# Kernel tuning notes

Measured on AMD Instinct MI355X. Metric: run time of the kernel, lower is better.

## Reference

```python
import jax, jax.numpy as jnp
import numpy as np

# Config mirroring the TF module: cross-attention path (one_on_rna == 2),
# use_attn_augument=1, aug_multiply=0, two_d_softm=1, two_d_softm_mul_row_count=1,
# reduce_level=20 (protok used for padding masks).
B, L, D, H = 4, 1024, 512, 8
DEPTH = D // H          # 64, matches the repeat(64) in padding_to_zeros
NEG = -1.0e9


def setup_inputs() -> dict:
    key = jax.random.key(0)
    ks = jax.random.split(key, 16)
    s = np.float32(1.0 / np.sqrt(D))  # glorot-ish scale
    q = jax.random.normal(ks[0], (B, L, D), jnp.float32)
    kv = jax.random.normal(ks[1], (B, L, D), jnp.float32)
    # protein tokens; 0 == padding (compared against 0.0 in the TF code)
    protok = jax.random.randint(ks[2], (B, L), 0, 21).astype(jnp.float32)
    statpot_hb = jax.random.uniform(ks[3], (B, L, L), dtype=jnp.float32)
    statpot_pi = jax.random.uniform(ks[4], (B, L, L), dtype=jnp.float32)
    # cross padding mask: 1.0 where the protein (query) position is padding
    pad = (protok == 0.0).astype(jnp.float32)            # [B, L]
    cross_mask = jnp.broadcast_to(pad[:, :, None], (B, L, L)).astype(jnp.float32)
    wq = jax.random.normal(ks[5], (D, D), jnp.float32) * s
    wk = jax.random.normal(ks[6], (D, D), jnp.float32) * s
    wv = jax.random.normal(ks[7], (D, D), jnp.float32) * s
    wo = jax.random.normal(ks[8], (D, D), jnp.float32) * s
    bq = jnp.zeros((D,), jnp.float32)
    bk = jnp.zeros((D,), jnp.float32)
    bv = jnp.zeros((D,), jnp.float32)
    bo = jnp.zeros((D,), jnp.float32)
    aug_weight_att = jnp.ones((1,), jnp.float32)
    aug_weight_aug = jnp.ones((1,), jnp.float32)
    return dict(q=q, kv=kv, protok=protok, statpot_hb=statpot_hb,
                statpot_pi=statpot_pi, cross_mask=cross_mask,
                wq=wq, bq=bq, wk=wk, bk=bk, wv=wv, bv=bv, wo=wo, bo=bo,
                aug_weight_att=aug_weight_att, aug_weight_aug=aug_weight_aug)


def _split_heads(x):
    # [B, L, D] -> [B, H, L, depth]
    return x.reshape(B, L, H, DEPTH).transpose(0, 2, 1, 3)


def reference(q, kv, protok, statpot_hb, statpot_pi, cross_mask,
              wq, bq, wk, bk, wv, bv, wo, bo, aug_weight_att, aug_weight_aug):
    # padding_to_zeros: zero features at padded protein positions
    pad_keep = (protok != 0.0).astype(q.dtype)[:, :, None]   # [B, L, 1]
    qp = (q @ wq + bq) * pad_keep   # query side is the protein (len == max_pro_len)
    k = kv @ wk + bk
    v = kv @ wv + bv
    qh, kh, vh = _split_heads(qp), _split_heads(k), _split_heads(v)

    # unscaled QK^T (original does NOT divide by sqrt(depth))
    logits = jnp.einsum('bhqd,bhkd->bhqk', qh, kh)           # [B,H,L,L]

    # statistical-potential augmentation (aug_multiply == 0 -> additive)
    table = jnp.stack([statpot_hb, statpot_pi], axis=1)      # [B,2,L,L]
    table = jnp.repeat(table, H // 2, axis=1)                # [B,H,L,L]
    logits = logits / jnp.max(logits)
    logits = aug_weight_att * logits
    table = aug_weight_aug * table
    table = table / jnp.max(table)
    logits = logits + table

    # additive large-negative mask, broadcast over heads
    logits = logits + cross_mask[:, None, :, :] * NEG

    # 2D softmax jointly over (query, key) axes
    attn = jax.nn.softmax(logits.reshape(B, H, L * L), axis=-1).reshape(B, H, L, L)

    # rescale by number of non-padded protein rows (two_d_softm_mul_row_count)
    mul = jnp.count_nonzero(protok, axis=1).astype(attn.dtype)[:, None, None, None]
    attn = attn * mul
    attn = attn / jnp.max(attn)

    # output = attn^T @ v : contracts the QUERY axis (as in the original matmul)
    out = jnp.einsum('bhqk,bhqd->bhkd', attn, vh)            # [B,H,L,depth]
    out = out.transpose(0, 2, 1, 3).reshape(B, L, D)
    out = out @ wo + bo
    out = out * pad_keep                                     # final padding zeroing
    return out
```

## Files before the change

### kernel.cpp

```cpp
#include <hip/hip_runtime.h>
#include <math.h>

#define BB 4
#define LL 1024
#define DD 512
#define HH 8
#define DEP 64
#define NEGV (-1.0e9f)

typedef __attribute__((ext_vector_type(8))) short bf16x8;
typedef __attribute__((ext_vector_type(4))) float f32x4;
typedef unsigned short u16;
typedef unsigned int u32;

#define S_TMAX 1
#define S_TMIN 2
#define S_MUL  4
#define S_SUM  8
#define S_M    40
#define P_TMAX 128
#define P_TMIN 384
#define P_GMAX 640
#define SCAL_F 1792
#define PER_T  (BB*HH*LL*DEP)

__device__ inline u16 f2b(float x) {
  u32 u = __float_as_uint(x);
  return (u16)((u + 0x7FFFu + ((u >> 16) & 1u)) >> 16);
}
__device__ inline float b2f(u16 h) { return __uint_as_float(((u32)h) << 16); }

__device__ inline void atomicMaxF(float* addr, float val) {
  unsigned int* ua = (unsigned int*)addr;
  unsigned int old = *ua;
  while (__uint_as_float(old) < val) {
    unsigned int assumed = old;
    old = atomicCAS(ua, assumed, __float_as_uint(val));
    if (old == assumed) break;
  }
}

__global__ __launch_bounds__(256) void k_tminmax(const float* __restrict__ hb,
                                                 const float* __restrict__ pi,
                                                 const float* __restrict__ protok,
                                                 float* __restrict__ ws) {
  const int t = threadIdx.x;
  if (blockIdx.x == 4 && t < 32) {
    ws[S_SUM + t] = 0.0f; ws[S_M + t] = -INFINITY;
  }
  if (blockIdx.x < 4) {
    int b = blockIdx.x;
    int cnt = 0;
    for (int l = t; l < LL; l += 256)
      cnt += (protok[b*LL + l] != 0.0f) ? 1 : 0;
    __shared__ int shc[4];
    int lane = t & 63, w = t >> 6;
    #pragma unroll
    for (int o = 32; o > 0; o >>= 1) cnt += __shfl_down(cnt, o);
    if (lane == 0) shc[w] = cnt;
    __syncthreads();
    if (t == 0) ws[S_MUL + b] = (float)(shc[0] + shc[1] + shc[2] + shc[3]);
  }
  const int g = blockIdx.x*256 + t;
  float mx = -INFINITY, mn = INFINITY;
  #pragma unroll
  for (int rep = 0; rep < 4; ++rep) {
    float4 a[4], c[4];
    #pragma unroll
    for (int j = 0; j < 4; ++j) {
      size_t idx = (size_t)rep*262144 + (size_t)j*65536 + g;
      a[j] = ((const float4*)hb)[idx];
      c[j] = ((const float4*)pi)[idx];
    }
    #pragma unroll
    for (int j = 0; j < 4; ++j) {
      mx = fmaxf(mx, fmaxf(fmaxf(a[j].x, a[j].y), fmaxf(a[j].z, a[j].w)));
      mx = fmaxf(mx, fmaxf(fmaxf(c[j].x, c[j].y), fmaxf(c[j].z, c[j].w)));
      mn = fminf(mn, fminf(fminf(a[j].x, a[j].y), fminf(a[j].z, a[j].w)));
      mn = fminf(mn, fminf(fminf(c[j].x, c[j].y), fminf(c[j].z, c[j].w)));
    }
  }
  __shared__ float shx[4], shn[4];
  int lane = t & 63, w = t >> 6;
  #pragma unroll
  for (int o = 32; o > 0; o >>= 1) {
    mx = fmaxf(mx, __shfl_down(mx, o));
    mn = fminf(mn, __shfl_down(mn, o));
  }
  if (lane == 0) { shx[w] = mx; shn[w] = mn; }
  __syncthreads();
  if (t == 0) {
    ws[P_TMAX + blockIdx.x] = fmaxf(fmaxf(shx[0], shx[1]), fmaxf(shx[2], shx[3]));
    ws[P_TMIN + blockIdx.x] = fminf(fminf(shn[0], shn[1]), fminf(shn[2], shn[3]));
  }
}

__global__ __launch_bounds__(256) void k_prep(
    const float* __restrict__ q, const float* __restrict__ kv,
    const float* __restrict__ wq, const float* __restrict__ wk,
    const float* __restrict__ wv, const float* __restrict__ wo,
    u16* __restrict__ Xb, u16* __restrict__ WTb, float* __restrict__ ws) {
  const int bid = blockIdx.x;
  const int t = threadIdx.x;
  if (bid < 2048) {
    int tg = bid*256 + t;
    int which = tg >> 18;
    size_t off8 = (size_t)(tg & 262143) * 8;
    const float* s = which ? kv : q;
    float4 f0 = *(const float4*)&s[off8];
    float4 f1 = *(const float4*)&s[off8 + 4];
    u32 p0 = (u32)f2b(f0.x) | ((u32)f2b(f0.y) << 16);
    u32 p1 = (u32)f2b(f0.z) | ((u32)f2b(f0.w) << 16);
    u32 p2 = (u32)f2b(f1.x) | ((u32)f2b(f1.y) << 16);
    u32 p3 = (u32)f2b(f1.z) | ((u32)f2b(f1.w) << 16);
    *(int4*)&Xb[(size_t)which*PER_T + off8] = make_int4(p0, p1, p2, p3);
  } else if (bid < 2304) {
    const int wid = bid - 2048;
    const int g = wid >> 6, rem = wid & 63;
    const int k0 = (rem >> 3)*64, n0 = (rem & 7)*64;
    const float* W = (g==0)?wq:(g==1)?wk:(g==2)?wv:wo;
    __shared__ u16 Ls[64][72];
    {
      const int r = t>>2, c16 = (t&3)*16;
      float v[16];
      #pragma unroll
      for (int j=0;j<4;++j) {
        float4 f = *(const float4*)&W[(size_t)(k0+r)*DD + n0 + c16 + 4*j];
        v[4*j]=f.x; v[4*j+1]=f.y; v[4*j+2]=f.z; v[4*j+3]=f.w;
      }
      u32 pk_[8];
      #pragma unroll
      for (int j=0;j<8;++j) pk_[j] = (u32)f2b(v[2*j]) | ((u32)f2b(v[2*j+1])<<16);
      *(int4*)&Ls[r][c16]   = make_int4(pk_[0],pk_[1],pk_[2],pk_[3]);
      *(int4*)&Ls[r][c16+8] = make_int4(pk_[4],pk_[5],pk_[6],pk_[7]);
    }
    __syncthreads();
    {
      const int n = t>>2, kk = (t&3)*16;
      u16 u[16];
      #pragma unroll
      for (int j=0;j<16;++j) u[j] = Ls[kk+j][n];
      u32 q_[8];
      #pragma unroll
      for (int j=0;j<8;++j) q_[j] = (u32)u[2*j] | ((u32)u[2*j+1]<<16);
      size_t dst = ((size_t)(g*DD + n0 + n))*DD + k0 + kk;
      *(int4*)&WTb[dst]   = make_int4(q_[0],q_[1],q_[2],q_[3]);
      *(int4*)&WTb[dst+8] = make_int4(q_[4],q_[5],q_[6],q_[7]);
    }
  } else {
    float tm = ws[P_TMAX + t];
    float tn = ws[P_TMIN + t];
    __shared__ float st[4], sn[4];
    int lane = t & 63, w = t >> 6;
    #pragma unroll
    for (int o = 32; o > 0; o >>= 1) {
      tm = fmaxf(tm, __shfl_down(tm, o));
      tn = fminf(tn, __shfl_down(tn, o));
    }
    if (lane == 0) { st[w] = tm; sn[w] = tn; }
    __syncthreads();
    if (t == 0) {
      ws[S_TMAX] = fmaxf(fmaxf(st[0], st[1]), fmaxf(st[2], st[3]));
      ws[S_TMIN] = fminf(fminf(sn[0], sn[1]), fminf(sn[2], sn[3]));
    }
  }
}

__global__ __launch_bounds__(256) void k1_proj(
    const float* __restrict__ protok,
    const float* __restrict__ bq, const float* __restrict__ bk,
    const float* __restrict__ bv,
    const u16* __restrict__ Xb, const u16* __restrict__ WTb,
    u16* __restrict__ QPb, u16* __restrict__ KHb, u16* __restrict__ VTb) {
  const int gid = blockIdx.z;
  const u16* X = Xb + (gid == 0 ? 0 : (size_t)PER_T);
  const float* bia = (gid == 0) ? bq : (gid == 1) ? bk : bv;
  const int m0 = blockIdx.x*64;
  const int h  = blockIdx.y;
  __shared__ u16 As[64][72];
  __shared__ u16 Bs[64][72];
  const int t = threadIdx.x;
  const int w = t>>6, lane = t&63, i = lane&15, g2 = lane>>4;
  const int sr = t>>2, sc = (t&3)*16;

  f32x4 acc[4];
  #pragma unroll
  for (int ct=0;ct<4;++ct) acc[ct] = (f32x4){0.f,0.f,0.f,0.f};

  for (int kk0 = 0; kk0 < DD; kk0 += 64) {
    __syncthreads();
    {
      size_t sx = (size_t)(m0+sr)*DD + kk0 + sc;
      *(int4*)&As[sr][sc]   = *(const int4*)&X[sx];
      *(int4*)&As[sr][sc+8] = *(const int4*)&X[sx+8];
    }
    {
      size_t src = ((size_t)(gid*DD + h*64 + sr))*DD + kk0 + sc;
      *(int4*)&Bs[sr][sc]   = *(const int4*)&WTb[src];
      *(int4*)&Bs[sr][sc+8] = *(const int4*)&WTb[src+8];
    }
    __syncthreads();
    bf16x8 a0 = *(const bf16x8*)&As[16*w + i][g2*8];
    bf16x8 a1 = *(const bf16x8*)&As[16*w + i][32 + g2*8];
    #pragma unroll
    for (int ct=0; ct<4; ++ct) {
      bf16x8 b0 = *(const bf16x8*)&Bs[ct*16 + i][g2*8];
      bf16x8 b1 = *(const bf16x8*)&Bs[ct*16 + i][32 + g2*8];
      acc[ct] = __builtin_amdgcn_mfma_f32_16x16x32_bf16(a0, b0, acc[ct], 0,0,0);
      acc[ct] = __builtin_amdgcn_mfma_f32_16x16x32_bf16(a1, b1, acc[ct], 0,0,0);
    }
  }
  __syncthreads();
  const int lrow = 16*w + g2*4;
  if (gid == 2) {
    #pragma unroll
    for (int ct=0;ct<4;++ct)
      #pragma unroll
      for (int r=0;r<4;++r)
        As[lrow + r][ct*16 + i] = f2b(acc[ct][r] + bia[h*64 + ct*16 + i]);
    __syncthreads();
    const int b = m0 >> 10, l0 = m0 & 1023;
    const int d = t>>2, lc = (t&3)*16;
    u16 u[16];
    #pragma unroll
    for (int j=0;j<16;++j) u[j] = As[lc+j][d];
    u32 q_[8];
    #pragma unroll
    for (int j=0;j<8;++j) q_[j] = (u32)u[2*j] | ((u32)u[2*j+1]<<16);
    size_t dst = ((size_t)(b*HH + h)*DEP + d)*LL + l0 + lc;
    *(int4*)&VTb[dst]   = make_int4(q_[0],q_[1],q_[2],q_[3]);
    *(int4*)&VTb[dst+8] = make_int4(q_[4],q_[5],q_[6],q_[7]);
  } else {
    u16* Y = (gid == 0) ? QPb : KHb;
    #pragma unroll
    for (int ct=0;ct<4;++ct)
      #pragma unroll
      for (int r=0;r<4;++r) {
        int m = m0 + lrow + r;
        float keep = (gid == 0) ? ((protok[m] != 0.0f) ? 1.0f : 0.0f) : 1.0f;
        int b = m >> 10, l = m & 1023;
        float val = (acc[ct][r] + bia[h*64 + ct*16 + i]) * keep;
        Y[((size_t)(b*HH + h)*LL + l)*DEP + ct*16 + i] = f2b(val);
      }
  }
}

__global__ __launch_bounds__(256) void k3_gmax(
    const u16* __restrict__ QPb, const u16* __restrict__ KHb,
    float* __restrict__ wsf) {
  const int q0 = blockIdx.x*128, bh = blockIdx.y, kz = blockIdx.z;
  __shared__ u16 Qs[2][64][72];
  __shared__ u16 Ks[2][64][72];
  const int t = threadIdx.x;
  const int w = t>>6, lane = t&63, i = lane&15, g2 = lane>>4;
  const int sr = t>>2, sc = (t&3)*16;
  const u16* Qb = QPb + (size_t)bh*LL*DEP;
  const u16* Kb = KHb + (size_t)bh*LL*DEP;
  #pragma unroll
  for (int qs = 0; qs < 2; ++qs) {
    size_t sq = (size_t)(q0 + qs*64 + sr)*DEP + sc;
    *(int4*)&Qs[qs][sr][sc]   = *(const int4*)&Qb[sq];
    *(int4*)&Qs[qs][sr][sc+8] = *(const int4*)&Qb[sq+8];
  }
  const int kb = kz*4;
  int4 rn0 = *(const int4*)&Kb[(size_t)(kb*64 + sr)*DEP + sc];
  int4 rn1 = *(const int4*)&Kb[(size_t)(kb*64 + sr)*DEP + sc + 8];
  __syncthreads();
  *(int4*)&Ks[0][sr][sc]   = rn0;
  *(int4*)&Ks[0][sr][sc+8] = rn1;
  rn0 = *(const int4*)&Kb[(size_t)((kb+1)*64 + sr)*DEP + sc];
  rn1 = *(const int4*)&Kb[(size_t)((kb+1)*64 + sr)*DEP + sc + 8];
  __syncthreads();
  bf16x8 a0[2], a1[2];
  #pragma unroll
  for (int qs = 0; qs < 2; ++qs) {
    a0[qs] = *(const bf16x8*)&Qs[qs][16*w + i][g2*8];
    a1[qs] = *(const bf16x8*)&Qs[qs][16*w + i][32 + g2*8];
  }
  float mx = -INFINITY;
  for (int kt = 0; kt < 4; ++kt) {
    const int cur = kt & 1;
    #pragma unroll
    for (int ct=0;ct<4;++ct) {
      bf16x8 b0 = *(const bf16x8*)&Ks[cur][ct*16 + i][g2*8];
      bf16x8 b1 = *(const bf16x8*)&Ks[cur][ct*16 + i][32 + g2*8];
      #pragma unroll
      for (int qs=0;qs<2;++qs) {
        f32x4 z = (f32x4){0.f,0.f,0.f,0.f};
        z = __builtin_amdgcn_mfma_f32_16x16x32_bf16(a0[qs], b0, z, 0,0,0);
        z = __builtin_amdgcn_mfma_f32_16x16x32_bf16(a1[qs], b1, z, 0,0,0);
        mx = fmaxf(mx, fmaxf(fmaxf(z[0],z[1]), fmaxf(z[2],z[3])));
      }
    }
    if (kt < 3) {
      __syncthreads();
      *(int4*)&Ks[cur^1][sr][sc]   = rn0;
      *(int4*)&Ks[cur^1][sr][sc+8] = rn1;
      if (kt < 2) {
        rn0 = *(const int4*)&Kb[(size_t)((kb+kt+2)*64 + sr)*DEP + sc];
        rn1 = *(const int4*)&Kb[(size_t)((kb+kt+2)*64 + sr)*DEP + sc + 8];
      }
      __syncthreads();
    }
  }
  __shared__ float red[4];
  #pragma unroll
  for (int o = 32; o > 0; o >>= 1) mx = fmaxf(mx, __shfl_down(mx, o));
  if (lane == 0) red[w] = mx;
  __syncthreads();
  if (t == 0)
    wsf[P_GMAX + (bh*8 + blockIdx.x)*4 + kz] =
        fmaxf(fmaxf(red[0],red[1]), fmaxf(red[2],red[3]));
}

__global__ __launch_bounds__(256) void k4_fused(
    const float* __restrict__ protok,
    const float* __restrict__ hb, const float* __restrict__ pi,
    const float* __restrict__ w_att, const float* __restrict__ w_aug,
    const u16* __restrict__ QPb, const u16* __restrict__ KHb,
    const u16* __restrict__ VTb,
    u16* __restrict__ Ob0, u16* __restrict__ Ob1,
    float* __restrict__ wsf) {
  const int k0 = blockIdx.x*64;
  const int bh = blockIdx.y, b = bh>>3, h = bh&7;
  const int qbase = blockIdx.z * 512;
  u16* Obz = blockIdx.z ? Ob1 : Ob0;
  const float* tab = ((h < 4) ? hb : pi) + (size_t)b*LL*LL;
  const int t = threadIdx.x;
  const int w = t>>6, lane = t&63, i = lane&15, g2 = lane>>4;
  const int sr = t>>2, sc = (t&3)*16;
  const int qlb = 16*w + g2*4;

  __shared__ float gsh;
  {
    float gm = -INFINITY;
    #pragma unroll
    for (int j=0;j<4;++j) gm = fmaxf(gm, wsf[P_GMAX + j*256 + t]);
    __shared__ float red[4];
    #pragma unroll
    for (int o = 32; o > 0; o >>= 1) gm = fmaxf(gm, __shfl_down(gm, o));
    if (lane == 0) red[w] = gm;
    __syncthreads();
    if (t == 0) gsh = fmaxf(fmaxf(red[0],red[1]), fmaxf(red[2],red[3]));
  }
  const float tmaxr = wsf[S_TMAX], tminr = wsf[S_TMIN];
  const float wa = w_att[0], wg = w_aug[0];
  const float tden = (wg >= 0.0f) ? (wg * tmaxr) : (wg * tminr);
  const float inv_t = wg / tden;

  __shared__ u16 Ks[64][72];
  __shared__ u16 Qs[64][72];
  __shared__ u16 Vt[64][72];
  __shared__ u16 Pt[64][72];
  {
    size_t sk = ((size_t)bh*LL + k0 + sr)*DEP + sc;
    *(int4*)&Ks[sr][sc]   = *(const int4*)&KHb[sk];
    *(int4*)&Ks[sr][sc+8] = *(const int4*)&KHb[sk+8];
  }
  int4 rq0 = *(const int4*)&QPb[((size_t)bh*LL + qbase + sr)*DEP + sc];
  int4 rq1 = *(const int4*)&QPb[((size_t)bh*LL + qbase + sr)*DEP + sc + 8];
  int4 rv0 = *(const int4*)&VTb[((size_t)bh*DEP + sr)*LL + qbase + sc];
  int4 rv1 = *(const int4*)&VTb[((size_t)bh*DEP + sr)*LL + qbase + sc + 8];
  float tvr[4][4];
  #pragma unroll
  for (int r=0;r<4;++r)
    #pragma unroll
    for (int ct=0;ct<4;++ct)
      tvr[r][ct] = tab[(size_t)(qbase + qlb + r)*LL + k0 + ct*16 + i];
  __syncthreads();
  const float inv_g = wa / gsh;
  bf16x8 kb0[4], kb1[4];
  #pragma unroll
  for (int ct=0;ct<4;++ct) {
    kb0[ct] = *(const bf16x8*)&Ks[ct*16 + i][g2*8];
    kb1[ct] = *(const bf16x8*)&Ks[ct*16 + i][32 + g2*8];
  }
  f32x4 accO[4];
  #pragma unroll
  for (int dt=0;dt<4;++dt) accO[dt] = (f32x4){0.f,0.f,0.f,0.f};
  float lsum = 0.0f, lmax = -INFINITY;

  for (int q0 = qbase; q0 < qbase + 512; q0 += 64) {
    const bool more = (q0 + 64) < (qbase + 512);
    __syncthreads();
    *(int4*)&Qs[sr][sc]   = rq0;
    *(int4*)&Qs[sr][sc+8] = rq1;
    *(int4*)&Vt[sr][sc]   = rv0;
    *(int4*)&Vt[sr][sc+8] = rv1;
    __syncthreads();
    if (more) {
      rq0 = *(const int4*)&QPb[((size_t)bh*LL + q0 + 64 + sr)*DEP + sc];
      rq1 = *(const int4*)&QPb[((size_t)bh*LL + q0 + 64 + sr)*DEP + sc + 8];
      rv0 = *(const int4*)&VTb[((size_t)bh*DEP + sr)*LL + q0 + 64 + sc];
      rv1 = *(const int4*)&VTb[((size_t)bh*DEP + sr)*LL + q0 + 64 + sc + 8];
    }
    bf16x8 a0 = *(const bf16x8*)&Qs[16*w + i][g2*8];
    bf16x8 a1 = *(const bf16x8*)&Qs[16*w + i][32 + g2*8];
    f32x4 s4[4];
    #pragma unroll
    for (int ct=0; ct<4; ++ct) {
      f32x4 z = (f32x4){0.f,0.f,0.f,0.f};
      z = __builtin_amdgcn_mfma_f32_16x16x32_bf16(a0, kb0[ct], z, 0,0,0);
      z = __builtin_amdgcn_mfma_f32_16x16x32_bf16(a1, kb1[ct], z, 0,0,0);
      s4[ct] = z;
    }
    float tv2[4][4];
    if (more) {
      #pragma unroll
      for (int r=0;r<4;++r)
        #pragma unroll
        for (int ct=0;ct<4;++ct)
          tv2[r][ct] = tab[(size_t)(q0 + 64 + qlb + r)*LL + k0 + ct*16 + i];
    }
    float madd[4];
    #pragma unroll
    for (int r=0;r<4;++r)
      madd[r] = (protok[b*LL + q0 + qlb + r] == 0.0f) ? NEGV : 0.0f;
    #pragma unroll
    for (int ct=0;ct<4;++ct) {
      float pr[4];
      #pragma unroll
      for (int r=0;r<4;++r) {
        float sp = fmaf(s4[ct][r], inv_g, fmaf(tvr[r][ct], inv_t, madd[r]));
        lmax = fmaxf(lmax, sp);
        float p = __expf(sp);
        lsum += p;
        pr[r] = p;
      }
      u32 pk0 = (u32)f2b(pr[0]) | ((u32)f2b(pr[1])<<16);
      u32 pk1 = (u32)f2b(pr[2]) | ((u32)f2b(pr[3])<<16);
      *(uint2*)&Pt[ct*16 + i][qlb] = make_uint2(pk0, pk1);
    }
    __syncthreads();
    bf16x8 pa0 = *(const bf16x8*)&Pt[16*w + i][g2*8];
    bf16x8 pa1 = *(const bf16x8*)&Pt[16*w + i][32 + g2*8];
    #pragma unroll
    for (int dt=0; dt<4; ++dt) {
      bf16x8 v0 = *(const bf16x8*)&Vt[dt*16 + i][g2*8];
      bf16x8 v1 = *(const bf16x8*)&Vt[dt*16 + i][32 + g2*8];
      accO[dt] = __builtin_amdgcn_mfma_f32_16x16x32_bf16(pa0, v0, accO[dt], 0,0,0);
      accO[dt] = __builtin_amdgcn_mfma_f32_16x16x32_bf16(pa1, v1, accO[dt], 0,0,0);
    }
    if (more) {
      #pragma unroll
      for (int r=0;r<4;++r)
        #pragma unroll
        for (int ct=0;ct<4;++ct) tvr[r][ct] = tv2[r][ct];
    }
  }
  #pragma unroll
  for (int dt=0;dt<4;++dt)
    #pragma unroll
    for (int r=0;r<4;++r)
      Obz[((size_t)bh*LL + k0 + qlb + r)*DEP + dt*16 + i] = f2b(accO[dt][r]);
  __shared__ float rs[4], rm[4];
  #pragma unroll
  for (int o = 32; o > 0; o >>= 1) {
    lsum += __shfl_down(lsum, o);
    lmax = fmaxf(lmax, __shfl_down(lmax, o));
  }
  if (lane == 0) { rs[w] = lsum; rm[w] = lmax; }
  __syncthreads();
  if (t == 0) {
    atomicAdd(&wsf[S_SUM + bh], rs[0]+rs[1]+rs[2]+rs[3]);
    atomicMaxF(&wsf[S_M + bh], fmaxf(fmaxf(rm[0], rm[1]), fmaxf(rm[2], rm[3])));
  }
}

__global__ __launch_bounds__(256) void k5_out(
    const float* __restrict__ protok,
    const float* __restrict__ bo,
    const u16* __restrict__ WTb,
    const u16* __restrict__ O0, const u16* __restrict__ O1,
    const float* __restrict__ wsf, float* __restrict__ out) {
  const int m0 = blockIdx.x*64, n0 = blockIdx.y*64;
  const int b = m0 >> 10, l0 = m0 & 1023;
  __shared__ u16 As[64][72];
  __shared__ u16 Bs[64][72];
  __shared__ float csh[8];
  const int t = threadIdx.x;
  const int w = t>>6, lane = t&63, i = lane&15, g2 = lane>>4;
  const int sr = t>>2, sc = (t&3)*16;

  __shared__ float ash[32];
  if (t < 32)
    ash[t] = wsf[S_MUL + (t>>3)] * __expf(wsf[S_M + t]) / wsf[S_SUM + t];
  __syncthreads();
  if (t < 8) {
    float amax = -INFINITY;
    #pragma unroll
    for (int j = 0; j < 32; ++j) amax = fmaxf(amax, ash[j]);
    csh[t] = (wsf[S_MUL + b] / wsf[S_SUM + b*HH + t]) / amax;
  }

  f32x4 acc[4];
  #pragma unroll
  for (int ct=0;ct<4;++ct) acc[ct] = (f32x4){0.f,0.f,0.f,0.f};

  for (int kk0 = 0; kk0 < DD; kk0 += 64) {
    const int h = kk0 >> 6;
    __syncthreads();
    {
      union { int4 v[2]; u16 u[16]; } u0, u1;
      size_t so = ((size_t)(b*HH + h)*LL + l0 + sr)*DEP + sc;
      u0.v[0] = *(const int4*)&O0[so];
      u0.v[1] = *(const int4*)&O0[so+8];
      u1.v[0] = *(const int4*)&O1[so];
      u1.v[1] = *(const int4*)&O1[so+8];
      const float cs = csh[h];
      u32 pk_[8];
      #pragma unroll
      for (int j=0;j<8;++j) {
        float lo = (b2f(u0.u[2*j])   + b2f(u1.u[2*j]))   * cs;
        float hi = (b2f(u0.u[2*j+1]) + b2f(u1.u[2*j+1])) * cs;
        pk_[j] = (u32)f2b(lo) | ((u32)f2b(hi)<<16);
      }
      *(int4*)&As[sr][sc]   = make_int4(pk_[0],pk_[1],pk_[2],pk_[3]);
      *(int4*)&As[sr][sc+8] = make_int4(pk_[4],pk_[5],pk_[6],pk_[7]);
    }
    {
      size_t src = ((size_t)(3*DD + n0 + sr))*DD + kk0 + sc;
      *(int4*)&Bs[sr][sc]   = *(const int4*)&WTb[src];
      *(int4*)&Bs[sr][sc+8] = *(const int4*)&WTb[src+8];
    }
    __syncthreads();
    bf16x8 a0 = *(const bf16x8*)&As[16*w + i][g2*8];
    bf16x8 a1 = *(const bf16x8*)&As[16*w + i][32 + g2*8];
    #pragma unroll
    for (int ct=0; ct<4; ++ct) {
      bf16x8 b0 = *(const bf16x8*)&Bs[ct*16 + i][g2*8];
      bf16x8 b1 = *(const bf16x8*)&Bs[ct*16 + i][32 + g2*8];
      acc[ct] = __builtin_amdgcn_mfma_f32_16x16x32_bf16(a0, b0, acc[ct], 0,0,0);
      acc[ct] = __builtin_amdgcn_mfma_f32_16x16x32_bf16(a1, b1, acc[ct], 0,0,0);
    }
  }
  #pragma unroll
  for (int ct=0;ct<4;++ct)
    #pragma unroll
    for (int r=0;r<4;++r) {
      int m = m0 + 16*w + g2*4 + r;
      float keep = (protok[m] != 0.0f) ? 1.0f : 0.0f;
      out[(size_t)m*DD + n0 + ct*16 + i] = (acc[ct][r] + bo[n0 + ct*16 + i]) * keep;
    }
}

extern "C" void kernel_launch(void* const* d_in, const int* in_sizes, int n_in,
                              void* d_out, int out_size, void* d_ws, size_t ws_size,
                              hipStream_t stream) {
  const float* q      = (const float*)d_in[0];
  const float* kv     = (const float*)d_in[1];
  const float* protok = (const float*)d_in[2];
  const float* hb     = (const float*)d_in[3];
  const float* pi     = (const float*)d_in[4];
  const float* wq = (const float*)d_in[6];
  const float* bq = (const float*)d_in[7];
  const float* wk = (const float*)d_in[8];
  const float* bk = (const float*)d_in[9];
  const float* wv = (const float*)d_in[10];
  const float* bv = (const float*)d_in[11];
  const float* wo = (const float*)d_in[12];
  const float* bo = (const float*)d_in[13];
  const float* w_att = (const float*)d_in[14];
  const float* w_aug = (const float*)d_in[15];
  float* wsf = (float*)d_ws;
  float* out = (float*)d_out;

  u16* base = (u16*)(wsf + SCAL_F);
  u16* QPb = base;
  u16* KHb = QPb + PER_T;
  u16* VTb = KHb + PER_T;
  u16* XO  = VTb + PER_T;
  u16* WTb = XO  + 2*PER_T;
  u16* Xb  = XO;
  u16* Ob0 = XO;
  u16* Ob1 = XO + PER_T;

  k_tminmax <<<256, 256, 0, stream>>>(hb, pi, protok, wsf);
  k_prep    <<<2305, 256, 0, stream>>>(q, kv, wq, wk, wv, wo, Xb, WTb, wsf);
  k1_proj   <<<dim3(64, 8, 3), 256, 0, stream>>>(protok, bq, bk, bv, Xb, WTb, QPb, KHb, VTb);
  k3_gmax   <<<dim3(8, 32, 4), 256, 0, stream>>>(QPb, KHb, wsf);
  k4_fused  <<<dim3(16, 32, 2), 256, 0, stream>>>(protok, hb, pi, w_att, w_aug,
                                                  QPb, KHb, VTb, Ob0, Ob1, wsf);
  k5_out    <<<dim3(64, 8), 256, 0, stream>>>(protok, bo, WTb, Ob0, Ob1, wsf, out);
}
```

Measured before the change: 215.3 us.

## Fuse table min/max into prep, drop LDS staging, unsplit query axis in attention

Merges the table min/max and row-count kernel into the prep kernel, which removes one launch and moves the final min/max reduction into the attention kernel. The projection and global-max kernels now load MFMA operands straight from global memory instead of staging them in LDS with barriers. The fused attention kernel stops splitting the query axis into two halves, so it writes a single output buffer and the output kernel no longer sums two partials. This halves attention grid parallelism and raises register pressure in exchange for less LDS traffic and fewer syncs.

```diff
diff --git a/kernel.cpp b/kernel.cpp
--- a/kernel.cpp
+++ b/kernel.cpp
@@ -40,65 +40,12 @@
   }
 }
 
-__global__ __launch_bounds__(256) void k_tminmax(const float* __restrict__ hb,
-                                                 const float* __restrict__ pi,
-                                                 const float* __restrict__ protok,
-                                                 float* __restrict__ ws) {
-  const int t = threadIdx.x;
-  if (blockIdx.x == 4 && t < 32) {
-    ws[S_SUM + t] = 0.0f; ws[S_M + t] = -INFINITY;
-  }
-  if (blockIdx.x < 4) {
-    int b = blockIdx.x;
-    int cnt = 0;
-    for (int l = t; l < LL; l += 256)
-      cnt += (protok[b*LL + l] != 0.0f) ? 1 : 0;
-    __shared__ int shc[4];
-    int lane = t & 63, w = t >> 6;
-    #pragma unroll
-    for (int o = 32; o > 0; o >>= 1) cnt += __shfl_down(cnt, o);
-    if (lane == 0) shc[w] = cnt;
-    __syncthreads();
-    if (t == 0) ws[S_MUL + b] = (float)(shc[0] + shc[1] + shc[2] + shc[3]);
-  }
-  const int g = blockIdx.x*256 + t;
-  float mx = -INFINITY, mn = INFINITY;
-  #pragma unroll
-  for (int rep = 0; rep < 4; ++rep) {
-    float4 a[4], c[4];
-    #pragma unroll
-    for (int j = 0; j < 4; ++j) {
-      size_t idx = (size_t)rep*262144 + (size_t)j*65536 + g;
-      a[j] = ((const float4*)hb)[idx];
-      c[j] = ((const float4*)pi)[idx];
-    }
-    #pragma unroll
-    for (int j = 0; j < 4; ++j) {
-      mx = fmaxf(mx, fmaxf(fmaxf(a[j].x, a[j].y), fmaxf(a[j].z, a[j].w)));
-      mx = fmaxf(mx, fmaxf(fmaxf(c[j].x, c[j].y), fmaxf(c[j].z, c[j].w)));
-      mn = fminf(mn, fminf(fminf(a[j].x, a[j].y), fminf(a[j].z, a[j].w)));
-      mn = fminf(mn, fminf(fminf(c[j].x, c[j].y), fminf(c[j].z, c[j].w)));
-    }
-  }
-  __shared__ float shx[4], shn[4];
-  int lane = t & 63, w = t >> 6;
-  #pragma unroll
-  for (int o = 32; o > 0; o >>= 1) {
-    mx = fmaxf(mx, __shfl_down(mx, o));
-    mn = fminf(mn, __shfl_down(mn, o));
-  }
-  if (lane == 0) { shx[w] = mx; shn[w] = mn; }
-  __syncthreads();
-  if (t == 0) {
-    ws[P_TMAX + blockIdx.x] = fmaxf(fmaxf(shx[0], shx[1]), fmaxf(shx[2], shx[3]));
-    ws[P_TMIN + blockIdx.x] = fminf(fminf(shn[0], shn[1]), fminf(shn[2], shn[3]));
-  }
-}
-
 __global__ __launch_bounds__(256) void k_prep(
     const float* __restrict__ q, const float* __restrict__ kv,
     const float* __restrict__ wq, const float* __restrict__ wk,
     const float* __restrict__ wv, const float* __restrict__ wo,
+    const float* __restrict__ hb, const float* __restrict__ pi,
+    const float* __restrict__ protok,
     u16* __restrict__ Xb, u16* __restrict__ WTb, float* __restrict__ ws) {
   const int bid = blockIdx.x;
   const int t = threadIdx.x;
@@ -147,22 +94,53 @@
       *(int4*)&WTb[dst]   = make_int4(q_[0],q_[1],q_[2],q_[3]);
       *(int4*)&WTb[dst+8] = make_int4(q_[4],q_[5],q_[6],q_[7]);
     }
+  } else if (bid < 2560) {
+    const int g = (bid - 2304)*256 + t;
+    float mx = -INFINITY, mn = INFINITY;
+    #pragma unroll
+    for (int rep = 0; rep < 4; ++rep) {
+      float4 a[4], c[4];
+      #pragma unroll
+      for (int j = 0; j < 4; ++j) {
+        size_t idx = (size_t)rep*262144 + (size_t)j*65536 + g;
+        a[j] = ((const float4*)hb)[idx];
+        c[j] = ((const float4*)pi)[idx];
+      }
+      #pragma unroll
+      for (int j = 0; j < 4; ++j) {
+        mx = fmaxf(mx, fmaxf(fmaxf(a[j].x, a[j].y), fmaxf(a[j].z, a[j].w)));
+        mx = fmaxf(mx, fmaxf(fmaxf(c[j].x, c[j].y), fmaxf(c[j].z, c[j].w)));
+        mn = fminf(mn, fminf(fminf(a[j].x, a[j].y), fminf(a[j].z, a[j].w)));
+        mn = fminf(mn, fminf(fminf(c[j].x, c[j].y), fminf(c[j].z, c[j].w)));
+      }
+    }
+    __shared__ float shx[4], shn[4];
+    int lane = t & 63, w = t >> 6;
+    #pragma unroll
+    for (int o = 32; o > 0; o >>= 1) {
+      mx = fmaxf(mx, __shfl_down(mx, o));
+      mn = fminf(mn, __shfl_down(mn, o));
+    }
+    if (lane == 0) { shx[w] = mx; shn[w] = mn; }
+    __syncthreads();
+    if (t == 0) {
+      ws[P_TMAX + bid - 2304] = fmaxf(fmaxf(shx[0], shx[1]), fmaxf(shx[2], shx[3]));
+      ws[P_TMIN + bid - 2304] = fminf(fminf(shn[0], shn[1]), fminf(shn[2], shn[3]));
+    }
+  } else if (bid < 2564) {
+    int b = bid - 2560;
+    int cnt = 0;
+    for (int l = t; l < LL; l += 256)
+      cnt += (protok[b*LL + l] != 0.0f) ? 1 : 0;
+    __shared__ int shc[4];
+    int lane = t & 63, w = t >> 6;
+    #pragma unroll
+    for (int o = 32; o > 0; o >>= 1) cnt += __shfl_down(cnt, o);
+    if (lane == 0) shc[w] = cnt;
+    __syncthreads();
+    if (t == 0) ws[S_MUL + b] = (float)(shc[0] + shc[1] + shc[2] + shc[3]);
   } else {
-    float tm = ws[P_TMAX + t];
-    float tn = ws[P_TMIN + t];
-    __shared__ float st[4], sn[4];
-    int lane = t & 63, w = t >> 6;
-    #pragma unroll
-    for (int o = 32; o > 0; o >>= 1) {
-      tm = fmaxf(tm, __shfl_down(tm, o));
-      tn = fminf(tn, __shfl_down(tn, o));
-    }
-    if (lane == 0) { st[w] = tm; sn[w] = tn; }
-    __syncthreads();
-    if (t == 0) {
-      ws[S_TMAX] = fmaxf(fmaxf(st[0], st[1]), fmaxf(st[2], st[3]));
-      ws[S_TMIN] = fminf(fminf(sn[0], sn[1]), fminf(sn[2], sn[3]));
-    }
+    if (t < 32) { ws[S_SUM + t] = 0.0f; ws[S_M + t] = -INFINITY; }
   }
 }
 
@@ -178,39 +156,28 @@
   const int m0 = blockIdx.x*64;
   const int h  = blockIdx.y;
   __shared__ u16 As[64][72];
-  __shared__ u16 Bs[64][72];
   const int t = threadIdx.x;
   const int w = t>>6, lane = t&63, i = lane&15, g2 = lane>>4;
-  const int sr = t>>2, sc = (t&3)*16;
+
+  const u16* Xr = X + (size_t)(m0 + 16*w + i)*DD;
+  const u16* Wb = WTb + ((size_t)gid*DD + h*64)*DD;
 
   f32x4 acc[4];
   #pragma unroll
   for (int ct=0;ct<4;++ct) acc[ct] = (f32x4){0.f,0.f,0.f,0.f};
 
+  #pragma unroll
   for (int kk0 = 0; kk0 < DD; kk0 += 64) {
-    __syncthreads();
-    {
-      size_t sx = (size_t)(m0+sr)*DD + kk0 + sc;
-      *(int4*)&As[sr][sc]   = *(const int4*)&X[sx];
-      *(int4*)&As[sr][sc+8] = *(const int4*)&X[sx+8];
-    }
-    {
-      size_t src = ((size_t)(gid*DD + h*64 + sr))*DD + kk0 + sc;
-      *(int4*)&Bs[sr][sc]   = *(const int4*)&WTb[src];
-      *(int4*)&Bs[sr][sc+8] = *(const int4*)&WTb[src+8];
-    }
-    __syncthreads();
-    bf16x8 a0 = *(const bf16x8*)&As[16*w + i][g2*8];
-    bf16x8 a1 = *(const bf16x8*)&As[16*w + i][32 + g2*8];
+    bf16x8 a0 = *(const bf16x8*)&Xr[kk0 + g2*8];
+    bf16x8 a1 = *(const bf16x8*)&Xr[kk0 + 32 + g2*8];
     #pragma unroll
     for (int ct=0; ct<4; ++ct) {
-      bf16x8 b0 = *(const bf16x8*)&Bs[ct*16 + i][g2*8];
-      bf16x8 b1 = *(const bf16x8*)&Bs[ct*16 + i][32 + g2*8];
+      bf16x8 b0 = *(const bf16x8*)&Wb[(size_t)(ct*16+i)*DD + kk0 + g2*8];
+      bf16x8 b1 = *(const bf16x8*)&Wb[(size_t)(ct*16+i)*DD + kk0 + 32 + g2*8];
       acc[ct] = __builtin_amdgcn_mfma_f32_16x16x32_bf16(a0, b0, acc[ct], 0,0,0);
       acc[ct] = __builtin_amdgcn_mfma_f32_16x16x32_bf16(a1, b1, acc[ct], 0,0,0);
     }
   }
-  __syncthreads();
   const int lrow = 16*w + g2*4;
   if (gid == 2) {
     #pragma unroll
@@ -248,59 +215,41 @@
 __global__ __launch_bounds__(256) void k3_gmax(
     const u16* __restrict__ QPb, const u16* __restrict__ KHb,
     float* __restrict__ wsf) {
-  const int q0 = blockIdx.x*128, bh = blockIdx.y, kz = blockIdx.z;
-  __shared__ u16 Qs[2][64][72];
-  __shared__ u16 Ks[2][64][72];
+  const int q0 = blockIdx.x*64, bh = blockIdx.y, kz = blockIdx.z;
   const int t = threadIdx.x;
   const int w = t>>6, lane = t&63, i = lane&15, g2 = lane>>4;
-  const int sr = t>>2, sc = (t&3)*16;
-  const u16* Qb = QPb + (size_t)bh*LL*DEP;
+  const u16* Qr = QPb + ((size_t)bh*LL + q0 + 16*w + i)*DEP;
+  bf16x8 aq0 = *(const bf16x8*)&Qr[g2*8];
+  bf16x8 aq1 = *(const bf16x8*)&Qr[32 + g2*8];
   const u16* Kb = KHb + (size_t)bh*LL*DEP;
-  #pragma unroll
-  for (int qs = 0; qs < 2; ++qs) {
-    size_t sq = (size_t)(q0 + qs*64 + sr)*DEP + sc;
-    *(int4*)&Qs[qs][sr][sc]   = *(const int4*)&Qb[sq];
-    *(int4*)&Qs[qs][sr][sc+8] = *(const int4*)&Qb[sq+8];
-  }
-  const int kb = kz*4;
-  int4 rn0 = *(const int4*)&Kb[(size_t)(kb*64 + sr)*DEP + sc];
-  int4 rn1 = *(const int4*)&Kb[(size_t)(kb*64 + sr)*DEP + sc + 8];
-  __syncthreads();
-  *(int4*)&Ks[0][sr][sc]   = rn0;
-  *(int4*)&Ks[0][sr][sc+8] = rn1;
-  rn0 = *(const int4*)&Kb[(size_t)((kb+1)*64 + sr)*DEP + sc];
-  rn1 = *(const int4*)&Kb[(size_t)((kb+1)*64 + sr)*DEP + sc + 8];
-  __syncthreads();
-  bf16x8 a0[2], a1[2];
-  #pragma unroll
-  for (int qs = 0; qs < 2; ++qs) {
-    a0[qs] = *(const bf16x8*)&Qs[qs][16*w + i][g2*8];
-    a1[qs] = *(const bf16x8*)&Qs[qs][16*w + i][32 + g2*8];
-  }
+  const int kbase = kz*512;
   float mx = -INFINITY;
-  for (int kt = 0; kt < 4; ++kt) {
-    const int cur = kt & 1;
+  bf16x8 c0[4], c1[4];
+  #pragma unroll
+  for (int ct=0;ct<4;++ct) {
+    c0[ct] = *(const bf16x8*)&Kb[(size_t)(kbase + ct*16+i)*DEP + g2*8];
+    c1[ct] = *(const bf16x8*)&Kb[(size_t)(kbase + ct*16+i)*DEP + 32 + g2*8];
+  }
+  #pragma unroll
+  for (int kt = 0; kt < 8; ++kt) {
+    bf16x8 n0[4], n1[4];
+    if (kt < 7) {
+      #pragma unroll
+      for (int ct=0;ct<4;++ct) {
+        n0[ct] = *(const bf16x8*)&Kb[(size_t)(kbase + (kt+1)*64 + ct*16+i)*DEP + g2*8];
+        n1[ct] = *(const bf16x8*)&Kb[(size_t)(kbase + (kt+1)*64 + ct*16+i)*DEP + 32 + g2*8];
+      }
+    }
     #pragma unroll
     for (int ct=0;ct<4;++ct) {
-      bf16x8 b0 = *(const bf16x8*)&Ks[cur][ct*16 + i][g2*8];
-      bf16x8 b1 = *(const bf16x8*)&Ks[cur][ct*16 + i][32 + g2*8];
-      #pragma unroll
-      for (int qs=0;qs<2;++qs) {
-        f32x4 z = (f32x4){0.f,0.f,0.f,0.f};
-        z = __builtin_amdgcn_mfma_f32_16x16x32_bf16(a0[qs], b0, z, 0,0,0);
-        z = __builtin_amdgcn_mfma_f32_16x16x32_bf16(a1[qs], b1, z, 0,0,0);
-        mx = fmaxf(mx, fmaxf(fmaxf(z[0],z[1]), fmaxf(z[2],z[3])));
-      }
-    }
-    if (kt < 3) {
-      __syncthreads();
-      *(int4*)&Ks[cur^1][sr][sc]   = rn0;
-      *(int4*)&Ks[cur^1][sr][sc+8] = rn1;
-      if (kt < 2) {
-        rn0 = *(const int4*)&Kb[(size_t)((kb+kt+2)*64 + sr)*DEP + sc];
-        rn1 = *(const int4*)&Kb[(size_t)((kb+kt+2)*64 + sr)*DEP + sc + 8];
-      }
-      __syncthreads();
+      f32x4 z = (f32x4){0.f,0.f,0.f,0.f};
+      z = __builtin_amdgcn_mfma_f32_16x16x32_bf16(aq0, c0[ct], z, 0,0,0);
+      z = __builtin_amdgcn_mfma_f32_16x16x32_bf16(aq1, c1[ct], z, 0,0,0);
+      mx = fmaxf(mx, fmaxf(fmaxf(z[0],z[1]), fmaxf(z[2],z[3])));
+    }
+    if (kt < 7) {
+      #pragma unroll
+      for (int ct=0;ct<4;++ct) { c0[ct] = n0[ct]; c1[ct] = n1[ct]; }
     }
   }
   __shared__ float red[4];
@@ -309,7 +258,7 @@
   if (lane == 0) red[w] = mx;
   __syncthreads();
   if (t == 0)
-    wsf[P_GMAX + (bh*8 + blockIdx.x)*4 + kz] =
+    wsf[P_GMAX + (bh*16 + blockIdx.x)*2 + kz] =
         fmaxf(fmaxf(red[0],red[1]), fmaxf(red[2],red[3]));
 }
 
@@ -318,94 +267,90 @@
     const float* __restrict__ hb, const float* __restrict__ pi,
     const float* __restrict__ w_att, const float* __restrict__ w_aug,
     const u16* __restrict__ QPb, const u16* __restrict__ KHb,
-    const u16* __restrict__ VTb,
-    u16* __restrict__ Ob0, u16* __restrict__ Ob1,
+    const u16* __restrict__ VTb, u16* __restrict__ Ob,
     float* __restrict__ wsf) {
   const int k0 = blockIdx.x*64;
   const int bh = blockIdx.y, b = bh>>3, h = bh&7;
-  const int qbase = blockIdx.z * 512;
-  u16* Obz = blockIdx.z ? Ob1 : Ob0;
   const float* tab = ((h < 4) ? hb : pi) + (size_t)b*LL*LL;
   const int t = threadIdx.x;
   const int w = t>>6, lane = t&63, i = lane&15, g2 = lane>>4;
-  const int sr = t>>2, sc = (t&3)*16;
   const int qlb = 16*w + g2*4;
 
-  __shared__ float gsh;
+  __shared__ u16 Pt[64][72];
+  __shared__ float Msk[1024];
+  __shared__ float rg[4], rt[4], rn[4];
+
   {
     float gm = -INFINITY;
     #pragma unroll
     for (int j=0;j<4;++j) gm = fmaxf(gm, wsf[P_GMAX + j*256 + t]);
-    __shared__ float red[4];
-    #pragma unroll
-    for (int o = 32; o > 0; o >>= 1) gm = fmaxf(gm, __shfl_down(gm, o));
-    if (lane == 0) red[w] = gm;
-    __syncthreads();
-    if (t == 0) gsh = fmaxf(fmaxf(red[0],red[1]), fmaxf(red[2],red[3]));
-  }
-  const float tmaxr = wsf[S_TMAX], tminr = wsf[S_TMIN];
+    float tm = wsf[P_TMAX + t], tn = wsf[P_TMIN + t];
+    #pragma unroll
+    for (int o = 32; o > 0; o >>= 1) {
+      gm = fmaxf(gm, __shfl_down(gm, o));
+      tm = fmaxf(tm, __shfl_down(tm, o));
+      tn = fminf(tn, __shfl_down(tn, o));
+    }
+    if (lane == 0) { rg[w] = gm; rt[w] = tm; rn[w] = tn; }
+  }
+  #pragma unroll
+  for (int j=0;j<4;++j) {
+    int l = j*256 + t;
+    Msk[l] = (protok[b*LL + l] == 0.0f) ? NEGV : 0.0f;
+  }
+  __syncthreads();
+  const float gmax  = fmaxf(fmaxf(rg[0],rg[1]), fmaxf(rg[2],rg[3]));
+  const float tmaxr = fmaxf(fmaxf(rt[0],rt[1]), fmaxf(rt[2],rt[3]));
+  const float tminr = fminf(fminf(rn[0],rn[1]), fminf(rn[2],rn[3]));
   const float wa = w_att[0], wg = w_aug[0];
+  const float inv_g = wa / gmax;
   const float tden = (wg >= 0.0f) ? (wg * tmaxr) : (wg * tminr);
   const float inv_t = wg / tden;
 
-  __shared__ u16 Ks[64][72];
-  __shared__ u16 Qs[64][72];
-  __shared__ u16 Vt[64][72];
-  __shared__ u16 Pt[64][72];
-  {
-    size_t sk = ((size_t)bh*LL + k0 + sr)*DEP + sc;
-    *(int4*)&Ks[sr][sc]   = *(const int4*)&KHb[sk];
-    *(int4*)&Ks[sr][sc+8] = *(const int4*)&KHb[sk+8];
-  }
-  int4 rq0 = *(const int4*)&QPb[((size_t)bh*LL + qbase + sr)*DEP + sc];
-  int4 rq1 = *(const int4*)&QPb[((size_t)bh*LL + qbase + sr)*DEP + sc + 8];
-  int4 rv0 = *(const int4*)&VTb[((size_t)bh*DEP + sr)*LL + qbase + sc];
-  int4 rv1 = *(const int4*)&VTb[((size_t)bh*DEP + sr)*LL + qbase + sc + 8];
+  const u16* Kr = KHb + ((size_t)bh*LL + k0)*DEP;
+  bf16x8 kb0[4], kb1[4];
+  #pragma unroll
+  for (int ct=0;ct<4;++ct) {
+    kb0[ct] = *(const bf16x8*)&Kr[(size_t)(ct*16+i)*DEP + g2*8];
+    kb1[ct] = *(const bf16x8*)&Kr[(size_t)(ct*16+i)*DEP + 32 + g2*8];
+  }
+  const u16* Qbase = QPb + (size_t)bh*LL*DEP;
+  const u16* Vbase = VTb + (size_t)bh*DEP*LL;
+  bf16x8 aq0 = *(const bf16x8*)&Qbase[(size_t)(16*w+i)*DEP + g2*8];
+  bf16x8 aq1 = *(const bf16x8*)&Qbase[(size_t)(16*w+i)*DEP + 32 + g2*8];
   float tvr[4][4];
   #pragma unroll
   for (int r=0;r<4;++r)
     #pragma unroll
     for (int ct=0;ct<4;++ct)
-      tvr[r][ct] = tab[(size_t)(qbase + qlb + r)*LL + k0 + ct*16 + i];
-  __syncthreads();
-  const float inv_g = wa / gsh;
-  bf16x8 kb0[4], kb1[4];
-  #pragma unroll
-  for (int ct=0;ct<4;++ct) {
-    kb0[ct] = *(const bf16x8*)&Ks[ct*16 + i][g2*8];
-    kb1[ct] = *(const bf16x8*)&Ks[ct*16 + i][32 + g2*8];
-  }
+      tvr[r][ct] = tab[(size_t)(qlb + r)*LL + k0 + ct*16 + i];
+
   f32x4 accO[4];
   #pragma unroll
   for (int dt=0;dt<4;++dt) accO[dt] = (f32x4){0.f,0.f,0.f,0.f};
   float lsum = 0.0f, lmax = -INFINITY;
 
-  for (int q0 = qbase; q0 < qbase + 512; q0 += 64) {
-    const bool more = (q0 + 64) < (qbase + 512);
-    __syncthreads();
-    *(int4*)&Qs[sr][sc]   = rq0;
-    *(int4*)&Qs[sr][sc+8] = rq1;
-    *(int4*)&Vt[sr][sc]   = rv0;
-    *(int4*)&Vt[sr][sc+8] = rv1;
-    __syncthreads();
-    if (more) {
-      rq0 = *(const int4*)&QPb[((size_t)bh*LL + q0 + 64 + sr)*DEP + sc];
-      rq1 = *(const int4*)&QPb[((size_t)bh*LL + q0 + 64 + sr)*DEP + sc + 8];
-      rv0 = *(const int4*)&VTb[((size_t)bh*DEP + sr)*LL + q0 + 64 + sc];
-      rv1 = *(const int4*)&VTb[((size_t)bh*DEP + sr)*LL + q0 + 64 + sc + 8];
-    }
-    bf16x8 a0 = *(const bf16x8*)&Qs[16*w + i][g2*8];
-    bf16x8 a1 = *(const bf16x8*)&Qs[16*w + i][32 + g2*8];
+  for (int q0 = 0; q0 < LL; q0 += 64) {
+    const bool more = (q0 + 64) < LL;
     f32x4 s4[4];
     #pragma unroll
     for (int ct=0; ct<4; ++ct) {
       f32x4 z = (f32x4){0.f,0.f,0.f,0.f};
-      z = __builtin_amdgcn_mfma_f32_16x16x32_bf16(a0, kb0[ct], z, 0,0,0);
-      z = __builtin_amdgcn_mfma_f32_16x16x32_bf16(a1, kb1[ct], z, 0,0,0);
+      z = __builtin_amdgcn_mfma_f32_16x16x32_bf16(aq0, kb0[ct], z, 0,0,0);
+      z = __builtin_amdgcn_mfma_f32_16x16x32_bf16(aq1, kb1[ct], z, 0,0,0);
       s4[ct] = z;
     }
+    bf16x8 vv0[4], vv1[4];
+    #pragma unroll
+    for (int dt=0;dt<4;++dt) {
+      vv0[dt] = *(const bf16x8*)&Vbase[(size_t)(dt*16+i)*LL + q0 + g2*8];
+      vv1[dt] = *(const bf16x8*)&Vbase[(size_t)(dt*16+i)*LL + q0 + 32 + g2*8];
+    }
+    bf16x8 aq0n, aq1n;
     float tv2[4][4];
     if (more) {
+      aq0n = *(const bf16x8*)&Qbase[(size_t)(q0+64+16*w+i)*DEP + g2*8];
+      aq1n = *(const bf16x8*)&Qbase[(size_t)(q0+64+16*w+i)*DEP + 32 + g2*8];
       #pragma unroll
       for (int r=0;r<4;++r)
         #pragma unroll
@@ -414,8 +359,8 @@
     }
     float madd[4];
     #pragma unroll
-    for (int r=0;r<4;++r)
-      madd[r] = (protok[b*LL + q0 + qlb + r] == 0.0f) ? NEGV : 0.0f;
+    for (int r=0;r<4;++r) madd[r] = Msk[q0 + qlb + r];
+    u32 pk_[4][2];
     #pragma unroll
     for (int ct=0;ct<4;++ct) {
       float pr[4];
@@ -427,21 +372,23 @@
         lsum += p;
         pr[r] = p;
       }
-      u32 pk0 = (u32)f2b(pr[0]) | ((u32)f2b(pr[1])<<16);
-      u32 pk1 = (u32)f2b(pr[2]) | ((u32)f2b(pr[3])<<16);
-      *(uint2*)&Pt[ct*16 + i][qlb] = make_uint2(pk0, pk1);
-    }
+      pk_[ct][0] = (u32)f2b(pr[0]) | ((u32)f2b(pr[1])<<16);
+      pk_[ct][1] = (u32)f2b(pr[2]) | ((u32)f2b(pr[3])<<16);
+    }
+    __syncthreads();
+    #pragma unroll
+    for (int ct=0;ct<4;++ct)
+      *(uint2*)&Pt[ct*16 + i][qlb] = make_uint2(pk_[ct][0], pk_[ct][1]);
     __syncthreads();
     bf16x8 pa0 = *(const bf16x8*)&Pt[16*w + i][g2*8];
     bf16x8 pa1 = *(const bf16x8*)&Pt[16*w + i][32 + g2*8];
     #pragma unroll
     for (int dt=0; dt<4; ++dt) {
-      bf16x8 v0 = *(const bf16x8*)&Vt[dt*16 + i][g2*8];
-      bf16x8 v1 = *(const bf16x8*)&Vt[dt*16 + i][32 + g2*8];
-      accO[dt] = __builtin_amdgcn_mfma_f32_16x16x32_bf16(pa0, v0, accO[dt], 0,0,0);
-      accO[dt] = __builtin_amdgcn_mfma_f32_16x16x32_bf16(pa1, v1, accO[dt], 0,0,0);
+      accO[dt] = __builtin_amdgcn_mfma_f32_16x16x32_bf16(pa0, vv0[dt], accO[dt], 0,0,0);
+      accO[dt] = __builtin_amdgcn_mfma_f32_16x16x32_bf16(pa1, vv1[dt], accO[dt], 0,0,0);
     }
     if (more) {
+      aq0 = aq0n; aq1 = aq1n;
       #pragma unroll
       for (int r=0;r<4;++r)
         #pragma unroll
@@ -452,7 +399,7 @@
   for (int dt=0;dt<4;++dt)
     #pragma unroll
     for (int r=0;r<4;++r)
-      Obz[((size_t)bh*LL + k0 + qlb + r)*DEP + dt*16 + i] = f2b(accO[dt][r]);
+      Ob[((size_t)bh*LL + k0 + qlb + r)*DEP + dt*16 + i] = f2b(accO[dt][r]);
   __shared__ float rs[4], rm[4];
   #pragma unroll
   for (int o = 32; o > 0; o >>= 1) {
@@ -470,8 +417,7 @@
 __global__ __launch_bounds__(256) void k5_out(
     const float* __restrict__ protok,
     const float* __restrict__ bo,
-    const u16* __restrict__ WTb,
-    const u16* __restrict__ O0, const u16* __restrict__ O1,
+    const u16* __restrict__ WTb, const u16* __restrict__ Ob,
     const float* __restrict__ wsf, float* __restrict__ out) {
   const int m0 = blockIdx.x*64, n0 = blockIdx.y*64;
   const int b = m0 >> 10, l0 = m0 & 1023;
@@ -501,20 +447,15 @@
     const int h = kk0 >> 6;
     __syncthreads();
     {
-      union { int4 v[2]; u16 u[16]; } u0, u1;
+      union { int4 v[2]; u16 u[16]; } uu;
       size_t so = ((size_t)(b*HH + h)*LL + l0 + sr)*DEP + sc;
-      u0.v[0] = *(const int4*)&O0[so];
-      u0.v[1] = *(const int4*)&O0[so+8];
-      u1.v[0] = *(const int4*)&O1[so];
-      u1.v[1] = *(const int4*)&O1[so+8];
+      uu.v[0] = *(const int4*)&Ob[so];
+      uu.v[1] = *(const int4*)&Ob[so+8];
       const float cs = csh[h];
       u32 pk_[8];
       #pragma unroll
-      for (int j=0;j<8;++j) {
-        float lo = (b2f(u0.u[2*j])   + b2f(u1.u[2*j]))   * cs;
-        float hi = (b2f(u0.u[2*j+1]) + b2f(u1.u[2*j+1])) * cs;
-        pk_[j] = (u32)f2b(lo) | ((u32)f2b(hi)<<16);
-      }
+      for (int j=0;j<8;++j)
+        pk_[j] = (u32)f2b(b2f(uu.u[2*j])*cs) | ((u32)f2b(b2f(uu.u[2*j+1])*cs)<<16);
       *(int4*)&As[sr][sc]   = make_int4(pk_[0],pk_[1],pk_[2],pk_[3]);
       *(int4*)&As[sr][sc+8] = make_int4(pk_[4],pk_[5],pk_[6],pk_[7]);
     }
@@ -572,14 +513,14 @@
   u16* XO  = VTb + PER_T;
   u16* WTb = XO  + 2*PER_T;
   u16* Xb  = XO;
-  u16* Ob0 = XO;
-  u16* Ob1 = XO + PER_T;
-
-  k_tminmax <<<256, 256, 0, stream>>>(hb, pi, protok, wsf);
-  k_prep    <<<2305, 256, 0, stream>>>(q, kv, wq, wk, wv, wo, Xb, WTb, wsf);
-  k1_proj   <<<dim3(64, 8, 3), 256, 0, stream>>>(protok, bq, bk, bv, Xb, WTb, QPb, KHb, VTb);
-  k3_gmax   <<<dim3(8, 32, 4), 256, 0, stream>>>(QPb, KHb, wsf);
-  k4_fused  <<<dim3(16, 32, 2), 256, 0, stream>>>(protok, hb, pi, w_att, w_aug,
-                                                  QPb, KHb, VTb, Ob0, Ob1, wsf);
-  k5_out    <<<dim3(64, 8), 256, 0, stream>>>(protok, bo, WTb, Ob0, Ob1, wsf, out);
-}
+  u16* Ob  = XO;
+
+  k_prep  <<<2565, 256, 0, stream>>>(q, kv, wq, wk, wv, wo, hb, pi, protok,
+                                     Xb, WTb, wsf);
+  k1_proj <<<dim3(64, 8, 3), 256, 0, stream>>>(protok, bq, bk, bv, Xb, WTb,
+                                               QPb, KHb, VTb);
+  k3_gmax <<<dim3(16, 32, 2), 256, 0, stream>>>(QPb, KHb, wsf);
+  k4_fused<<<dim3(16, 32), 256, 0, stream>>>(protok, hb, pi, w_att, w_aug,
+                                             QPb, KHb, VTb, Ob, wsf);
+  k5_out  <<<dim3(64, 8), 256, 0, stream>>>(protok, bo, WTb, Ob, wsf, out);
+}
```

Measured after the change: 283.9 us. 31.8% more time.
